# Kernel optimization log

Measured on AMD Instinct MI355X. Metric: run time of the kernel, lower is better.

## Reference

```python
import jax, jax.numpy as jnp
import numpy as np

N, N_OBS, D, HID = 200000, 100000, 32, 128

def setup_inputs() -> dict:
    key = jax.random.key(0)
    ks = jax.random.split(key, 24)
    p = lambda k, shp: jax.random.normal(k, shp, dtype=jnp.float32) * 0.05
    inp = {
        "current_time": jnp.ones((1, 1), dtype=jnp.float32),
        "mgn_h": jax.random.normal(ks[0], (N, HID), dtype=jnp.float32),
        "X_obs": jax.random.normal(ks[1], (N_OBS, D), dtype=jnp.float32),
        "M_obs": (jax.random.uniform(ks[2], (N_OBS, D)) < 0.5).astype(jnp.float32),
        "i_obs": jnp.arange(N_OBS, dtype=jnp.int32),  # unique, in-range row ids
        "last_x": jax.random.normal(ks[3], (N, D), dtype=jnp.float32),
        "last_t": jax.random.uniform(ks[4], (N, D), dtype=jnp.float32),
        "W_gx": p(ks[5], (D, D)),
        "W_gh": p(ks[6], (HID, D)),
        "Wz": p(ks[7], (D, HID)), "Vz": p(ks[8], (D, HID)), "Uz": p(ks[9], (HID, HID)), "bz": jnp.zeros((HID,), jnp.float32),
        "Wr": p(ks[10], (D, HID)), "Vr": p(ks[11], (D, HID)), "Ur": p(ks[12], (HID, HID)), "br": jnp.zeros((HID,), jnp.float32),
        "Wh": p(ks[13], (D, HID)), "Vh": p(ks[14], (D, HID)), "Uh": p(ks[15], (HID, HID)), "bh": jnp.zeros((HID,), jnp.float32),
    }
    return inp


def reference(current_time, mgn_h, X_obs, M_obs, i_obs, last_x, last_t,
              W_gx, W_gh, Wz, Vz, Uz, bz, Wr, Vr, Ur, br, Wh, Vh, Uh, bh):
    # --- masked scatter update of last observed values ---
    last_x = last_x.at[i_obs].set(last_x[i_obs] * (1.0 - M_obs) + X_obs * M_obs)
    # mean over observed rows (faithful to original: numerator sums raw X_obs)
    mean_x = jnp.sum(X_obs, axis=0, keepdims=True) / jnp.sum(M_obs + 1e-6, axis=0, keepdims=True)
    interval = current_time - last_t                       # [N, D]
    last_t = last_t.at[i_obs].set(last_t[i_obs] * (1.0 - M_obs) + current_time * M_obs)
    # decay gates (torch Linear: x @ W.T, no bias)
    gamma_x = jnp.exp(-jax.nn.relu(interval @ W_gx.T))      # [N, D]
    gamma_h = jnp.exp(-jax.nn.relu(interval @ W_gh.T))      # [N, HID]
    gx = gamma_x[i_obs]                                     # [n_obs, D]
    X_hat = (M_obs * X_obs
             + (1.0 - M_obs) * gx * last_x[i_obs]
             + (1.0 - M_obs) * (1.0 - gx) * mean_x)
    # --- GRU-D cell on observed rows ---
    h = gamma_h[i_obs] * mgn_h[i_obs]                       # decayed hidden [n_obs, HID]
    z = jax.nn.sigmoid(X_hat @ Wz + M_obs @ Vz + h @ Uz + bz)
    r = jax.nn.sigmoid(X_hat @ Wr + M_obs @ Vr + h @ Ur + br)
    h_tilde = jnp.tanh(X_hat @ Wh + M_obs @ Vh + (r * h) @ Uh + bh)
    h_new = (1.0 - z) * h + z * h_tilde
    mgn_h = mgn_h.at[i_obs].set(h_new)
    return mgn_h, last_x, last_t
```

## Files before the change

### kernel.cpp

```cpp
#include <hip/hip_runtime.h>
#include <hip/hip_bf16.h>

#define D_ 32
#define HID_ 128
#define ROWS 32
#define NCOPY 1024
#define NB_Z 25
#define NB_P 308
#define NB_M 512

typedef __attribute__((ext_vector_type(8))) short bf16x8;
typedef __attribute__((ext_vector_type(4))) float f32x4;
typedef __attribute__((ext_vector_type(4))) unsigned short us4;

__device__ __forceinline__ unsigned short bfh(float v) {
    __hip_bfloat16 b = __float2bfloat16(v);
    unsigned short u;
    __builtin_memcpy(&u, &b, 2);
    return u;
}
__device__ __forceinline__ float bfh2f(unsigned short u) {
    return __uint_as_float(((unsigned)u) << 16);
}
__device__ __forceinline__ float fsig(float x) {
    return __fdividef(1.0f, 1.0f + __expf(-x));
}
__device__ __forceinline__ float ftanh(float x) {
    return 1.0f - __fdividef(2.0f, __expf(2.0f * x) + 1.0f);
}

__global__ __launch_bounds__(256) void kA(
    unsigned* __restrict__ bm, int nwords,
    const float* __restrict__ W_gx, const float* __restrict__ W_gh,
    const float* __restrict__ Wz, const float* __restrict__ Vz, const float* __restrict__ Uz,
    const float* __restrict__ Wr, const float* __restrict__ Vr, const float* __restrict__ Ur,
    const float* __restrict__ Wh, const float* __restrict__ Vh, const float* __restrict__ Uh,
    short* __restrict__ gxh, short* __restrict__ gxl,
    short* __restrict__ ghh, short* __restrict__ ghl,
    short* __restrict__ zrh, short* __restrict__ zrl,
    short* __restrict__ h3h, short* __restrict__ h3l,
    const float* __restrict__ X_obs, const float* __restrict__ M_obs,
    float* __restrict__ partials, int n_obs, int chunk)
{
    __shared__ float4 rx[32][9], rm[32][9];
    int bid = blockIdx.x;
    if (bid < NB_Z) {
        int i = bid * 256 + threadIdx.x;
        if (i < nwords) bm[i] = 0u;
        return;
    }
    if (bid < NB_Z + NB_P) {
        int tid = (bid - NB_Z) * 256 + threadIdx.x;
        if (tid >= 78848) return;
        float v = 0.f;
        short* ph;
        short* pl;
        int local;
        if (tid < 1024) {
            local = tid;
            int j = local & 7, lane = (local >> 3) & 63, tn = local >> 9;
            int k = ((lane >> 4) << 3) + j;
            int n = tn * 16 + (lane & 15);
            v = W_gx[n * D_ + k];
            ph = gxh; pl = gxl;
        } else if (tid < 5120) {
            local = tid - 1024;
            int j = local & 7, lane = (local >> 3) & 63, tn = local >> 9;
            int k = ((lane >> 4) << 3) + j;
            int n = tn * 16 + (lane & 15);
            v = W_gh[n * D_ + k];
            ph = ghh; pl = ghl;
        } else if (tid < 54272) {
            local = tid - 5120;
            int j = local & 7, lane = (local >> 3) & 63, fs = local >> 9;
            int ks = fs % 6, tn = fs / 6;
            int k = ks * 32 + ((lane >> 4) << 3) + j;
            int n = tn * 16 + (lane & 15);
            const float *W, *V, *U;
            int nc;
            if (n < 128) { W = Wz; V = Vz; U = Uz; nc = n; }
            else         { W = Wr; V = Vr; U = Ur; nc = n - 128; }
            if (k < 32)       v = W[k * HID_ + nc];
            else if (k < 64)  v = V[(k - 32) * HID_ + nc];
            else              v = U[(k - 64) * HID_ + nc];
            ph = zrh; pl = zrl;
        } else {
            local = tid - 54272;
            int j = local & 7, lane = (local >> 3) & 63, fs = local >> 9;
            int ks = fs % 6, tn = fs / 6;
            int k = ks * 32 + ((lane >> 4) << 3) + j;
            int n = tn * 16 + (lane & 15);
            if (k < 32)       v = Wh[k * HID_ + n];
            else if (k < 64)  v = Vh[(k - 32) * HID_ + n];
            else              v = Uh[(k - 64) * HID_ + n];
            ph = h3h; pl = h3l;
        }
        unsigned short hi = bfh(v);
        unsigned short lo = bfh(v - bfh2f(hi));
        ph[local] = (short)hi;
        pl[local] = (short)lo;
        return;
    }
    int mb = bid - (NB_Z + NB_P);
    int start = mb * chunk;
    int end = start + chunk;
    if (end > n_obs) end = n_obs;
    int rq = threadIdx.x >> 3, c4 = threadIdx.x & 7;
    float4 sx = make_float4(0.f, 0.f, 0.f, 0.f);
    float4 sm = sx;
    for (int j = start + rq; j < end; j += 32) {
        float4 xv = ((const float4*)X_obs)[j * 8 + c4];
        float4 mv = ((const float4*)M_obs)[j * 8 + c4];
        sx.x += xv.x; sx.y += xv.y; sx.z += xv.z; sx.w += xv.w;
        sm.x += mv.x + 1e-6f; sm.y += mv.y + 1e-6f; sm.z += mv.z + 1e-6f; sm.w += mv.w + 1e-6f;
    }
    rx[rq][c4] = sx;
    rm[rq][c4] = sm;
    __syncthreads();
    #pragma unroll
    for (int off = 16; off >= 1; off >>= 1) {
        if (rq < off) {
            float4 a = rx[rq][c4], b = rx[rq + off][c4];
            a.x += b.x; a.y += b.y; a.z += b.z; a.w += b.w;
            rx[rq][c4] = a;
            float4 c = rm[rq][c4], d = rm[rq + off][c4];
            c.x += d.x; c.y += d.y; c.z += d.z; c.w += d.w;
            rm[rq][c4] = c;
        }
        __syncthreads();
    }
    if (threadIdx.x < 8) {
        *(float4*)&partials[mb * 64 + threadIdx.x * 4]      = rx[0][threadIdx.x];
        *(float4*)&partials[mb * 64 + 32 + threadIdx.x * 4] = rm[0][threadIdx.x];
    }
}

__global__ __launch_bounds__(256) void kB(
    const int* __restrict__ i_obs, unsigned* __restrict__ bm, int n_obs, int nbB,
    const float* __restrict__ partials, float* __restrict__ mean_x)
{
    __shared__ float red[4][64];
    int bid = blockIdx.x;
    if (bid < nbB) {
        int i = bid * 256 + threadIdx.x;
        if (i < n_obs) {
            int gi = i_obs[i];
            atomicOr(&bm[gi >> 5], 1u << (gi & 31));
        }
        return;
    }
    int t = threadIdx.x;
    int s = t >> 6, d = t & 63;
    float acc = 0.f;
    for (int b = s; b < NB_M; b += 4) acc += partials[b * 64 + d];
    red[s][d] = acc;
    __syncthreads();
    if (t < 64) red[0][t] = red[0][t] + red[1][t] + red[2][t] + red[3][t];
    __syncthreads();
    if (t < 32) mean_x[t] = red[0][t] / red[0][t + 32];
}

__global__ __launch_bounds__(512, 8) void k_fused(
    const float* __restrict__ ct_p,
    const float* __restrict__ mgn_h,
    const float* __restrict__ X_obs,
    const float* __restrict__ M_obs,
    const int*   __restrict__ i_obs,
    const float* __restrict__ last_x,
    const float* __restrict__ last_t,
    const float* __restrict__ bz, const float* __restrict__ br, const float* __restrict__ bh,
    const float* __restrict__ mean_x,
    const short* __restrict__ gxh, const short* __restrict__ gxl,
    const short* __restrict__ ghh, const short* __restrict__ ghl,
    const short* __restrict__ zrh, const short* __restrict__ zrl,
    const short* __restrict__ h3h, const short* __restrict__ h3l,
    const unsigned* __restrict__ bm,
    float* __restrict__ out_h, float* __restrict__ out_lx, float* __restrict__ out_lt,
    int n_obs, int N, int nblk)
{
    __shared__ unsigned short sh_h_hi[ROWS][136], sh_h_lo[ROWS][136];
    __shared__ unsigned short sh_ivxh_hi[ROWS][40], sh_ivxh_lo[ROWS][40];
    __shared__ unsigned short sh_M[ROWS][40];
    __shared__ float s_lxn[ROWS][33];
    __shared__ float s_mean[D_];
    __shared__ int   s_idx[ROWS];

    const int t = threadIdx.x;
    const int bid = blockIdx.x;

    if (bid >= nblk) {
        int rid = bid - nblk;
        long nh = (long)N * (HID_ / 4);
        long nx = (long)N * (D_ / 4);
        long total = nh + 2 * nx;
        const float4* s_mgn_g = (const float4*)mgn_h;
        const float4* s_lx_g  = (const float4*)last_x;
        const float4* s_lt_g  = (const float4*)last_t;
        float4* d_h  = (float4*)out_h;
        float4* d_lx = (float4*)out_lx;
        float4* d_lt = (float4*)out_lt;
        for (long i = (long)rid * 512 + t; i < total; i += (long)NCOPY * 512) {
            if (i < nh) {
                int row = (int)(i >> 5);
                if (!((bm[row >> 5] >> (row & 31)) & 1u)) d_h[i] = s_mgn_g[i];
            } else if (i < nh + nx) {
                long j = i - nh;
                int row = (int)(j >> 3);
                if (!((bm[row >> 5] >> (row & 31)) & 1u)) d_lx[j] = s_lx_g[j];
            } else {
                long j = i - nh - nx;
                int row = (int)(j >> 3);
                if (!((bm[row >> 5] >> (row & 31)) & 1u)) d_lt[j] = s_lt_g[j];
            }
        }
        return;
    }

    const int row0 = bid * ROWS;
    const int wave = t >> 6, lane = t & 63;
    const int lo4 = lane & 15, hi2 = lane >> 4;

    if (t < ROWS) {
        int j = row0 + t;
        s_idx[t] = (j < n_obs) ? i_obs[j] : -1;
    }
    if (t >= 64 && t < 96) s_mean[t - 64] = mean_x[t - 64];
    __syncthreads();
    const float ctv = ct_p[0];

    float hreg[2][4];
    {
        int c = wave * 16 + lo4;
        #pragma unroll
        for (int si = 0; si < 2; si++) {
            #pragma unroll
            for (int q = 0; q < 4; q++) {
                int r = si * 16 + hi2 * 4 + q;
                int gi = s_idx[r];
                hreg[si][q] = (gi >= 0) ? mgn_h[(long)gi * HID_ + c] : 0.f;
            }
        }
    }

    if (t < 256) {
        int rr = t >> 3, c4 = t & 7, d0 = c4 * 4;
        int gi = s_idx[rr];
        float4 Mm = make_float4(0.f, 0.f, 0.f, 0.f);
        float4 itv = Mm, lxn = Mm;
        if (gi >= 0) {
            int j = row0 + rr;
            float4 Xv = ((const float4*)X_obs)[j * 8 + c4];
            Mm = ((const float4*)M_obs)[j * 8 + c4];
            float4 lx = ((const float4*)last_x)[(long)gi * 8 + c4];
            float4 lt = ((const float4*)last_t)[(long)gi * 8 + c4];
            float4 ltn;
            itv.x = ctv - lt.x; lxn.x = lx.x * (1.f - Mm.x) + Xv.x * Mm.x; ltn.x = lt.x * (1.f - Mm.x) + ctv * Mm.x;
            itv.y = ctv - lt.y; lxn.y = lx.y * (1.f - Mm.y) + Xv.y * Mm.y; ltn.y = lt.y * (1.f - Mm.y) + ctv * Mm.y;
            itv.z = ctv - lt.z; lxn.z = lx.z * (1.f - Mm.z) + Xv.z * Mm.z; ltn.z = lt.z * (1.f - Mm.z) + ctv * Mm.z;
            itv.w = ctv - lt.w; lxn.w = lx.w * (1.f - Mm.w) + Xv.w * Mm.w; ltn.w = lt.w * (1.f - Mm.w) + ctv * Mm.w;
            ((float4*)out_lx)[(long)gi * 8 + c4] = lxn;
            ((float4*)out_lt)[(long)gi * 8 + c4] = ltn;
        }
        us4 ih, il, mh;
        {
            unsigned short h0 = bfh(itv.x); ih.x = h0; il.x = bfh(itv.x - bfh2f(h0)); mh.x = bfh(Mm.x);
            unsigned short h1 = bfh(itv.y); ih.y = h1; il.y = bfh(itv.y - bfh2f(h1)); mh.y = bfh(Mm.y);
            unsigned short h2 = bfh(itv.z); ih.z = h2; il.z = bfh(itv.z - bfh2f(h2)); mh.z = bfh(Mm.z);
            unsigned short h3 = bfh(itv.w); ih.w = h3; il.w = bfh(itv.w - bfh2f(h3)); mh.w = bfh(Mm.w);
        }
        *(us4*)&sh_ivxh_hi[rr][d0] = ih;
        *(us4*)&sh_ivxh_lo[rr][d0] = il;
        *(us4*)&sh_M[rr][d0]       = mh;
        s_lxn[rr][d0 + 0] = lxn.x; s_lxn[rr][d0 + 1] = lxn.y; s_lxn[rr][d0 + 2] = lxn.z; s_lxn[rr][d0 + 3] = lxn.w;
    }
    __syncthreads();

    const bf16x8* vgxh = (const bf16x8*)gxh;
    const bf16x8* vgxl = (const bf16x8*)gxl;
    const bf16x8* vghh = (const bf16x8*)ghh;
    const bf16x8* vghl = (const bf16x8*)ghl;
    const bf16x8* vzrh = (const bf16x8*)zrh;
    const bf16x8* vzrl = (const bf16x8*)zrl;
    const bf16x8* vh3h = (const bf16x8*)h3h;
    const bf16x8* vh3l = (const bf16x8*)h3l;

    {
        bf16x8 bhi = vghh[wave * 64 + lane];
        bf16x8 blo = vghl[wave * 64 + lane];
        int c = wave * 16 + lo4;
        #pragma unroll
        for (int si = 0; si < 2; si++) {
            int ar = si * 16 + lo4;
            bf16x8 ahi = *(const bf16x8*)&sh_ivxh_hi[ar][hi2 * 8];
            bf16x8 alo = *(const bf16x8*)&sh_ivxh_lo[ar][hi2 * 8];
            f32x4 acc = {0.f, 0.f, 0.f, 0.f};
            acc = __builtin_amdgcn_mfma_f32_16x16x32_bf16(ahi, bhi, acc, 0, 0, 0);
            acc = __builtin_amdgcn_mfma_f32_16x16x32_bf16(ahi, blo, acc, 0, 0, 0);
            acc = __builtin_amdgcn_mfma_f32_16x16x32_bf16(alo, bhi, acc, 0, 0, 0);
            #pragma unroll
            for (int q = 0; q < 4; q++) {
                int r = si * 16 + hi2 * 4 + q;
                float g = __expf(-fmaxf(acc[q], 0.f));
                float hv = g * hreg[si][q];
                hreg[si][q] = hv;
                unsigned short hh = bfh(hv);
                sh_h_hi[r][c] = hh;
                sh_h_lo[r][c] = bfh(hv - bfh2f(hh));
            }
        }
    }
    f32x4 gxacc[2];
    if (wave < 2) {
        bf16x8 bhi = vgxh[wave * 64 + lane];
        bf16x8 blo = vgxl[wave * 64 + lane];
        #pragma unroll
        for (int si = 0; si < 2; si++) {
            int ar = si * 16 + lo4;
            bf16x8 ahi = *(const bf16x8*)&sh_ivxh_hi[ar][hi2 * 8];
            bf16x8 alo = *(const bf16x8*)&sh_ivxh_lo[ar][hi2 * 8];
            f32x4 acc = {0.f, 0.f, 0.f, 0.f};
            acc = __builtin_amdgcn_mfma_f32_16x16x32_bf16(ahi, bhi, acc, 0, 0, 0);
            acc = __builtin_amdgcn_mfma_f32_16x16x32_bf16(ahi, blo, acc, 0, 0, 0);
            acc = __builtin_amdgcn_mfma_f32_16x16x32_bf16(alo, bhi, acc, 0, 0, 0);
            gxacc[si] = acc;
        }
    }
    __syncthreads();

    if (wave < 2) {
        int c = wave * 16 + lo4;
        float mn2 = s_mean[c];
        #pragma unroll
        for (int si = 0; si < 2; si++) {
            #pragma unroll
            for (int q = 0; q < 4; q++) {
                int r = si * 16 + hi2 * 4 + q;
                float g = __expf(-fmaxf(gxacc[si][q], 0.f));
                float Mv = bfh2f(sh_M[r][c]);
                float lx = s_lxn[r][c];
                float xh = lx * (Mv + (1.f - Mv) * g) + (1.f - Mv) * (1.f - g) * mn2;
                unsigned short xhh = bfh(xh);
                sh_ivxh_hi[r][c] = xhh;
                sh_ivxh_lo[r][c] = bfh(xh - bfh2f(xhh));
            }
        }
    }
    __syncthreads();

    f32x4 accA[2][2];
    #pragma unroll
    for (int ti = 0; ti < 2; ti++)
        #pragma unroll
        for (int si = 0; si < 2; si++)
            accA[ti][si] = (f32x4){0.f, 0.f, 0.f, 0.f};

    #pragma unroll
    for (int ks = 0; ks < 6; ks++) {
        bf16x8 Ah[2], Al[2];
        bool hasLo = (ks != 1);
        #pragma unroll
        for (int si = 0; si < 2; si++) {
            int ar = si * 16 + lo4;
            if (ks == 0) {
                Ah[si] = *(const bf16x8*)&sh_ivxh_hi[ar][hi2 * 8];
                Al[si] = *(const bf16x8*)&sh_ivxh_lo[ar][hi2 * 8];
            } else if (ks == 1) {
                Ah[si] = *(const bf16x8*)&sh_M[ar][hi2 * 8];
                Al[si] = Ah[si];
            } else {
                int ko = (ks - 2) * 32 + hi2 * 8;
                Ah[si] = *(const bf16x8*)&sh_h_hi[ar][ko];
                Al[si] = *(const bf16x8*)&sh_h_lo[ar][ko];
            }
        }
        #pragma unroll
        for (int ti = 0; ti < 2; ti++) {
            int tn = wave + ti * 8;
            int slot = (tn * 6 + ks) * 64 + lane;
            bf16x8 bhi = vzrh[slot];
            bf16x8 blo = vzrl[slot];
            #pragma unroll
            for (int si = 0; si < 2; si++) {
                f32x4 a = accA[ti][si];
                a = __builtin_amdgcn_mfma_f32_16x16x32_bf16(Ah[si], bhi, a, 0, 0, 0);
                a = __builtin_amdgcn_mfma_f32_16x16x32_bf16(Ah[si], blo, a, 0, 0, 0);
                if (hasLo)
                    a = __builtin_amdgcn_mfma_f32_16x16x32_bf16(Al[si], bhi, a, 0, 0, 0);
                accA[ti][si] = a;
            }
        }
    }
    float zreg[2][4], rreg[2][4];
    {
        int c = wave * 16 + lo4;
        float bzv = bz[c], brv = br[c];
        #pragma unroll
        for (int si = 0; si < 2; si++)
            #pragma unroll
            for (int q = 0; q < 4; q++) {
                zreg[si][q] = fsig(accA[0][si][q] + bzv);
                rreg[si][q] = fsig(accA[1][si][q] + brv);
            }
    }
    __syncthreads();

    {
        int c = wave * 16 + lo4;
        #pragma unroll
        for (int si = 0; si < 2; si++) {
            #pragma unroll
            for (int q = 0; q < 4; q++) {
                int r = si * 16 + hi2 * 4 + q;
                float rh = rreg[si][q] * hreg[si][q];
                unsigned short rhh = bfh(rh);
                sh_h_hi[r][c] = rhh;
                sh_h_lo[r][c] = bfh(rh - bfh2f(rhh));
            }
        }
    }
    __syncthreads();

    f32x4 accB[2];
    #pragma unroll
    for (int si = 0; si < 2; si++)
        accB[si] = (f32x4){0.f, 0.f, 0.f, 0.f};

    #pragma unroll
    for (int ks = 0; ks < 6; ks++) {
        bf16x8 Ah[2], Al[2];
        bool hasLo = (ks != 1);
        #pragma unroll
        for (int si = 0; si < 2; si++) {
            int ar = si * 16 + lo4;
            if (ks == 0) {
                Ah[si] = *(const bf16x8*)&sh_ivxh_hi[ar][hi2 * 8];
                Al[si] = *(const bf16x8*)&sh_ivxh_lo[ar][hi2 * 8];
            } else if (ks == 1) {
                Ah[si] = *(const bf16x8*)&sh_M[ar][hi2 * 8];
                Al[si] = Ah[si];
            } else {
                int ko = (ks - 2) * 32 + hi2 * 8;
                Ah[si] = *(const bf16x8*)&sh_h_hi[ar][ko];
                Al[si] = *(const bf16x8*)&sh_h_lo[ar][ko];
            }
        }
        int slot = (wave * 6 + ks) * 64 + lane;
        bf16x8 bhi = vh3h[slot];
        bf16x8 blo = vh3l[slot];
        #pragma unroll
        for (int si = 0; si < 2; si++) {
            f32x4 a = accB[si];
            a = __builtin_amdgcn_mfma_f32_16x16x32_bf16(Ah[si], bhi, a, 0, 0, 0);
            a = __builtin_amdgcn_mfma_f32_16x16x32_bf16(Ah[si], blo, a, 0, 0, 0);
            if (hasLo)
                a = __builtin_amdgcn_mfma_f32_16x16x32_bf16(Al[si], bhi, a, 0, 0, 0);
            accB[si] = a;
        }
    }
    {
        int c = wave * 16 + lo4;
        float bhv = bh[c];
        #pragma unroll
        for (int si = 0; si < 2; si++) {
            #pragma unroll
            for (int q = 0; q < 4; q++) {
                int r = si * 16 + hi2 * 4 + q;
                int gi = s_idx[r];
                if (gi < 0) continue;
                float ht = ftanh(accB[si][q] + bhv);
                float z  = zreg[si][q];
                out_h[(long)gi * HID_ + c] = (1.f - z) * hreg[si][q] + z * ht;
            }
        }
    }
}

extern "C" void kernel_launch(void* const* d_in, const int* in_sizes, int n_in,
                              void* d_out, int out_size, void* d_ws, size_t ws_size,
                              hipStream_t stream)
{
    const float* ct     = (const float*)d_in[0];
    const float* mgn_h  = (const float*)d_in[1];
    const float* X_obs  = (const float*)d_in[2];
    const float* M_obs  = (const float*)d_in[3];
    const int*   i_obs  = (const int*)d_in[4];
    const float* last_x = (const float*)d_in[5];
    const float* last_t = (const float*)d_in[6];
    const float* W_gx   = (const float*)d_in[7];
    const float* W_gh   = (const float*)d_in[8];
    const float* Wz = (const float*)d_in[9];
    const float* Vz = (const float*)d_in[10];
    const float* Uz = (const float*)d_in[11];
    const float* bz = (const float*)d_in[12];
    const float* Wr = (const float*)d_in[13];
    const float* Vr = (const float*)d_in[14];
    const float* Ur = (const float*)d_in[15];
    const float* br = (const float*)d_in[16];
    const float* Wh = (const float*)d_in[17];
    const float* Vh = (const float*)d_in[18];
    const float* Uh = (const float*)d_in[19];
    const float* bh = (const float*)d_in[20];

    int n_obs = in_sizes[4];
    int N = in_sizes[1] / HID_;

    float* out_h  = (float*)d_out;
    float* out_lx = out_h + (long)N * HID_;
    float* out_lt = out_lx + (long)N * D_;

    char* w = (char*)d_ws;
    float* partials = (float*)w;
    float* mean_x   = (float*)(w + 131072);
    short* gxh = (short*)(w + 131200);
    short* gxl = (short*)(w + 133248);
    short* ghh = (short*)(w + 135296);
    short* ghl = (short*)(w + 143488);
    short* zrh = (short*)(w + 151680);
    short* zrl = (short*)(w + 249984);
    short* h3h = (short*)(w + 348288);
    short* h3l = (short*)(w + 397440);
    unsigned* bm = (unsigned*)(w + 446592);

    int nwords = (N + 31) / 32;
    int chunk = (n_obs + NB_M - 1) / NB_M;
    kA<<<NB_Z + NB_P + NB_M, 256, 0, stream>>>(
        bm, nwords,
        W_gx, W_gh, Wz, Vz, Uz, Wr, Vr, Ur, Wh, Vh, Uh,
        gxh, gxl, ghh, ghl, zrh, zrl, h3h, h3l,
        X_obs, M_obs, partials, n_obs, chunk);

    int nbB = (n_obs + 255) / 256;
    kB<<<nbB + 1, 256, 0, stream>>>(i_obs, bm, n_obs, nbB, partials, mean_x);

    int nblk = (n_obs + ROWS - 1) / ROWS;
    k_fused<<<nblk + NCOPY, 512, 0, stream>>>(
        ct, mgn_h, X_obs, M_obs, i_obs, last_x, last_t,
        bz, br, bh, mean_x,
        gxh, gxl, ghh, ghl, zrh, zrl, h3h, h3l,
        bm, out_h, out_lx, out_lt, n_obs, N, nblk);
}
```

Measured before the change: 158.6 us.

## Interleave copy and compute blocks in fused kernel; move bitmap build into kA

Clearing the observed-row bitmap now happens in a hipMemsetAsync, and setting its bits moves from kB into kA, so kB becomes a single-block mean reduction. In the fused kernel, copy blocks are interleaved one in four with GRU compute blocks instead of all being placed after them. This is meant to overlap bandwidth-bound copying with compute-bound work across the device and to shorten kB. It adds a memset launch and some idle blocks when nblk is smaller than three times NCOPY.

```diff
diff --git a/kernel.cpp b/kernel.cpp
--- a/kernel.cpp
+++ b/kernel.cpp
@@ -5,7 +5,6 @@
 #define HID_ 128
 #define ROWS 32
 #define NCOPY 1024
-#define NB_Z 25
 #define NB_P 308
 #define NB_M 512
 
@@ -30,7 +29,7 @@
 }
 
 __global__ __launch_bounds__(256) void kA(
-    unsigned* __restrict__ bm, int nwords,
+    const int* __restrict__ i_obs, unsigned* __restrict__ bm, int nbB,
     const float* __restrict__ W_gx, const float* __restrict__ W_gh,
     const float* __restrict__ Wz, const float* __restrict__ Vz, const float* __restrict__ Uz,
     const float* __restrict__ Wr, const float* __restrict__ Vr, const float* __restrict__ Ur,
@@ -44,13 +43,16 @@
 {
     __shared__ float4 rx[32][9], rm[32][9];
     int bid = blockIdx.x;
-    if (bid < NB_Z) {
+    if (bid < nbB) {
         int i = bid * 256 + threadIdx.x;
-        if (i < nwords) bm[i] = 0u;
+        if (i < n_obs) {
+            int gi = i_obs[i];
+            atomicOr(&bm[gi >> 5], 1u << (gi & 31));
+        }
         return;
     }
-    if (bid < NB_Z + NB_P) {
-        int tid = (bid - NB_Z) * 256 + threadIdx.x;
+    if (bid < nbB + NB_P) {
+        int tid = (bid - nbB) * 256 + threadIdx.x;
         if (tid >= 78848) return;
         float v = 0.f;
         short* ph;
@@ -101,7 +103,7 @@
         pl[local] = (short)lo;
         return;
     }
-    int mb = bid - (NB_Z + NB_P);
+    int mb = bid - (nbB + NB_P);
     int start = mb * chunk;
     int end = start + chunk;
     if (end > n_obs) end = n_obs;
@@ -136,19 +138,9 @@
 }
 
 __global__ __launch_bounds__(256) void kB(
-    const int* __restrict__ i_obs, unsigned* __restrict__ bm, int n_obs, int nbB,
     const float* __restrict__ partials, float* __restrict__ mean_x)
 {
     __shared__ float red[4][64];
-    int bid = blockIdx.x;
-    if (bid < nbB) {
-        int i = bid * 256 + threadIdx.x;
-        if (i < n_obs) {
-            int gi = i_obs[i];
-            atomicOr(&bm[gi >> 5], 1u << (gi & 31));
-        }
-        return;
-    }
     int t = threadIdx.x;
     int s = t >> 6, d = t & 63;
     float acc = 0.f;
@@ -188,8 +180,17 @@
     const int t = threadIdx.x;
     const int bid = blockIdx.x;
 
-    if (bid >= nblk) {
-        int rid = bid - nblk;
+    bool isCopy = false;
+    int rid;
+    const int inter = 4 * NCOPY;
+    if (bid < inter) {
+        if ((bid & 3) == 3) { isCopy = true; rid = bid >> 2; }
+        else                {                rid = (bid >> 2) * 3 + (bid & 3); }
+    } else {
+        rid = 3 * NCOPY + (bid - inter);
+    }
+
+    if (isCopy) {
         long nh = (long)N * (HID_ / 4);
         long nx = (long)N * (D_ / 4);
         long total = nh + 2 * nx;
@@ -215,8 +216,9 @@
         }
         return;
     }
-
-    const int row0 = bid * ROWS;
+    if (rid >= nblk) return;
+
+    const int row0 = rid * ROWS;
     const int wave = t >> 6, lane = t & 63;
     const int lo4 = lane & 15, hi2 = lane >> 4;
 
@@ -522,18 +524,21 @@
     unsigned* bm = (unsigned*)(w + 446592);
 
     int nwords = (N + 31) / 32;
+    hipMemsetAsync(bm, 0, (size_t)nwords * 4, stream);
+
+    int nbB = (n_obs + 255) / 256;
     int chunk = (n_obs + NB_M - 1) / NB_M;
-    kA<<<NB_Z + NB_P + NB_M, 256, 0, stream>>>(
-        bm, nwords,
+    kA<<<nbB + NB_P + NB_M, 256, 0, stream>>>(
+        i_obs, bm, nbB,
         W_gx, W_gh, Wz, Vz, Uz, Wr, Vr, Ur, Wh, Vh, Uh,
         gxh, gxl, ghh, ghl, zrh, zrl, h3h, h3l,
         X_obs, M_obs, partials, n_obs, chunk);
 
-    int nbB = (n_obs + 255) / 256;
-    kB<<<nbB + 1, 256, 0, stream>>>(i_obs, bm, n_obs, nbB, partials, mean_x);
+    kB<<<1, 256, 0, stream>>>(partials, mean_x);
 
     int nblk = (n_obs + ROWS - 1) / ROWS;
-    k_fused<<<nblk + NCOPY, 512, 0, stream>>>(
+    int grid = (nblk > 3 * NCOPY) ? (nblk + NCOPY) : (4 * NCOPY);
+    k_fused<<<grid, 512, 0, stream>>>(
         ct, mgn_h, X_obs, M_obs, i_obs, last_x, last_t,
         bz, br, bh, mean_x,
         gxh, gxl, ghh, ghl, zrh, zrl, h3h, h3l,
```

New measurement: 168.3 us. 6.1% more time.
